# Performance work log

Hardware: AMD Instinct MI355X
Metric: run time of the kernel (lower is better)

The kernel has to match this reference:

```python
import jax, jax.numpy as jnp
import numpy as np

B, C, L = 4, 64, 4096

def setup_inputs() -> dict:
    key = jax.random.key(0)
    ks = jax.random.split(key, 7)
    s = 1.0 / np.sqrt(C)
    return {
        "x": jax.random.normal(ks[0], (B, C, L), dtype=jnp.float32),
        "wq": jax.random.uniform(ks[1], (C, C), jnp.float32, -s, s),
        "bq": jax.random.uniform(ks[2], (C,), jnp.float32, -s, s),
        "wk": jax.random.uniform(ks[3], (C, C), jnp.float32, -s, s),
        "bk": jax.random.uniform(ks[4], (C,), jnp.float32, -s, s),
        "wv": jax.random.uniform(ks[5], (C, C), jnp.float32, -s, s),
        "bv": jax.random.uniform(ks[6], (C,), jnp.float32, -s, s),
    }

def reference(x, wq, bq, wk, bk, wv, bv):
    # x: [B, C, L]; conv1d kernel-size-1 == per-position linear over channels.
    scale = jnp.sqrt(jnp.asarray(x.shape[1], x.dtype))
    # project and move to [B, L, C]
    q = jnp.einsum('oc,bcl->blo', wq, x) + bq  # [B, L, C]
    k = jnp.einsum('oc,bcl->blo', wk, x) + bk
    v = jnp.einsum('oc,bcl->blo', wv, x) + bv
    attn = jnp.einsum('bic,bjc->bij', q, k) / scale  # [B, L, L]
    attn = jax.nn.softmax(attn, axis=-1)
    out = jnp.einsum('bij,bjc->bic', attn, v)  # [B, L, C]
    return out.transpose(0, 2, 1) + x  # back to [B, C, L] with residual
```

## Files before the change

kernel.cpp:

```cpp
#include <hip/hip_runtime.h>
#include <hip/hip_bf16.h>

typedef float    f32x4  __attribute__((ext_vector_type(4)));
typedef float    f32x16 __attribute__((ext_vector_type(16)));
typedef short    s16x4  __attribute__((ext_vector_type(4)));
typedef short    s16x8  __attribute__((ext_vector_type(8)));
typedef unsigned u32x4  __attribute__((ext_vector_type(4)));
typedef __bf16   bf16x8 __attribute__((ext_vector_type(8)));

#define DEVI __device__ __forceinline__

DEVI short f2bf(float f) {
    unsigned u = __builtin_bit_cast(unsigned, f);
    u += 0x8000u;
    return (short)(u >> 16);
}
DEVI unsigned cvt_pk_bf16(float lo, float hi) {
#if defined(__HIP_DEVICE_COMPILE__)
    unsigned r;
    asm("v_cvt_pk_bf16_f32 %0, %1, %2" : "=v"(r) : "v"(lo), "v"(hi));
    return r;
#else
    return (unsigned)(unsigned short)f2bf(lo) | ((unsigned)(unsigned short)f2bf(hi) << 16);
#endif
}

DEVI float fast_exp2(float x) {
#if defined(__HIP_DEVICE_COMPILE__) && __has_builtin(__builtin_amdgcn_exp2f)
    return __builtin_amdgcn_exp2f(x);
#else
    return exp2f(x);
#endif
}

DEVI f32x4 mfma32(s16x8 a, s16x8 b, f32x4 c) {
#if defined(__HIP_DEVICE_COMPILE__) && __has_builtin(__builtin_amdgcn_mfma_f32_16x16x32_bf16)
    return __builtin_amdgcn_mfma_f32_16x16x32_bf16(
        __builtin_bit_cast(bf16x8, a), __builtin_bit_cast(bf16x8, b), c, 0, 0, 0);
#else
    asm volatile("v_mfma_f32_16x16x32_bf16 %0, %1, %2, %0" : "+v"(c) : "v"(a), "v"(b));
    return c;
#endif
}

DEVI f32x16 mfma3216(s16x8 a, s16x8 b, f32x16 c) {
#if defined(__HIP_DEVICE_COMPILE__) && __has_builtin(__builtin_amdgcn_mfma_f32_32x32x16_bf16)
    return __builtin_amdgcn_mfma_f32_32x32x16_bf16(
        __builtin_bit_cast(bf16x8, a), __builtin_bit_cast(bf16x8, b), c, 0, 0, 0);
#else
    asm volatile("v_mfma_f32_32x32x16_bf16 %0, %1, %2, %0" : "+v"(c) : "v"(a), "v"(b));
    return c;
#endif
}

DEVI void setprio1() {
#if defined(__HIP_DEVICE_COMPILE__)
    __builtin_amdgcn_s_setprio(1);
#endif
}
DEVI void setprio0() {
#if defined(__HIP_DEVICE_COMPILE__)
    __builtin_amdgcn_s_setprio(0);
#endif
}

DEVI void gld_lds16(const short* g, short* ldsb, int lane) {
#if defined(__HIP_DEVICE_COMPILE__) && __has_builtin(__builtin_amdgcn_global_load_lds)
    __builtin_amdgcn_global_load_lds(
        (const __attribute__((address_space(1))) void*)g,
        (__attribute__((address_space(3))) void*)ldsb, 16, 0, 0);
#else
    *reinterpret_cast<s16x8*>(ldsb + lane * 8) =
        *reinterpret_cast<const s16x8*>(g);
#endif
}

__global__ __launch_bounds__(512) void qkv_proj(
    const float* __restrict__ x,
    const float* __restrict__ wq, const float* __restrict__ bq,
    const float* __restrict__ wk, const float* __restrict__ bk,
    const float* __restrict__ wv, const float* __restrict__ bv,
    short* __restrict__ Qg, short* __restrict__ Kp, short* __restrict__ Vp)
{
    __shared__ short Xt[32 * 64];

    const int b  = blockIdx.x >> 7;
    const int l0 = (blockIdx.x & 127) * 32;
    const int t  = threadIdx.x;
    const float QS = 0.18033688011112042f;

    {
        const int c  = t & 63;
        const int lh = (t >> 6) * 4;
        const float* xr = x + ((size_t)b * 64 + c) * 4096 + l0 + lh;
        const float4 x0 = *reinterpret_cast<const float4*>(xr);
        float xv[4] = {x0.x, x0.y, x0.z, x0.w};
        #pragma unroll
        for (int i = 0; i < 4; ++i) {
            const int l = lh + i;
            Xt[l * 64 + (((c >> 3) ^ (l & 7)) * 8) + (c & 7)] = f2bf(xv[i]);
        }
    }

    const int lane = t & 63, w = t >> 6;
    const int g = lane >> 4, col = lane & 15;
    const int o0 = (w & 3) * 16;
    const int h  = w >> 2;

    s16x8 wqf[2], wkf[2], wvf[2];
    #pragma unroll
    for (int kc = 0; kc < 2; ++kc) {
        const int cb = 8 * g + 32 * kc;
        const float4 q0 = *reinterpret_cast<const float4*>(wq + (o0 + col) * 64 + cb);
        const float4 q1 = *reinterpret_cast<const float4*>(wq + (o0 + col) * 64 + cb + 4);
        const float4 k0 = *reinterpret_cast<const float4*>(wk + (o0 + col) * 64 + cb);
        const float4 k1 = *reinterpret_cast<const float4*>(wk + (o0 + col) * 64 + cb + 4);
        const float4 v0 = *reinterpret_cast<const float4*>(wv + (o0 + col) * 64 + cb);
        const float4 v1 = *reinterpret_cast<const float4*>(wv + (o0 + col) * 64 + cb + 4);
        wqf[kc][0] = f2bf(q0.x * QS); wqf[kc][1] = f2bf(q0.y * QS);
        wqf[kc][2] = f2bf(q0.z * QS); wqf[kc][3] = f2bf(q0.w * QS);
        wqf[kc][4] = f2bf(q1.x * QS); wqf[kc][5] = f2bf(q1.y * QS);
        wqf[kc][6] = f2bf(q1.z * QS); wqf[kc][7] = f2bf(q1.w * QS);
        wkf[kc][0] = f2bf(k0.x); wkf[kc][1] = f2bf(k0.y);
        wkf[kc][2] = f2bf(k0.z); wkf[kc][3] = f2bf(k0.w);
        wkf[kc][4] = f2bf(k1.x); wkf[kc][5] = f2bf(k1.y);
        wkf[kc][6] = f2bf(k1.z); wkf[kc][7] = f2bf(k1.w);
        wvf[kc][0] = f2bf(v0.x); wvf[kc][1] = f2bf(v0.y);
        wvf[kc][2] = f2bf(v0.z); wvf[kc][3] = f2bf(v0.w);
        wvf[kc][4] = f2bf(v1.x); wvf[kc][5] = f2bf(v1.y);
        wvf[kc][6] = f2bf(v1.z); wvf[kc][7] = f2bf(v1.w);
    }
    const f32x4 bq4 = *reinterpret_cast<const f32x4*>(bq + o0 + 4 * g);
    const f32x4 bk4 = *reinterpret_cast<const f32x4*>(bk + o0 + 4 * g);
    const float bvs = bv[o0 + col];

    __syncthreads();

    {
        const int row = h * 16 + col;
        const s16x8 xf0 = *reinterpret_cast<const s16x8*>(
            &Xt[row * 64 + ((g ^ (row & 7)) * 8)]);
        const s16x8 xf1 = *reinterpret_cast<const s16x8*>(
            &Xt[row * 64 + (((g + 4) ^ (row & 7)) * 8)]);

        f32x4 qa = bq4 * QS;
        qa = mfma32(wqf[0], xf0, qa);
        qa = mfma32(wqf[1], xf1, qa);
        f32x4 ka = bk4;
        ka = mfma32(wkf[0], xf0, ka);
        ka = mfma32(wkf[1], xf1, ka);
        f32x4 va = {bvs, bvs, bvs, bvs};
        va = mfma32(xf0, wvf[0], va);
        va = mfma32(xf1, wvf[1], va);

        s16x4 qs, ks;
        #pragma unroll
        for (int r = 0; r < 4; ++r) { qs[r] = f2bf(qa[r]); ks[r] = f2bf(ka[r]); }

        const int l  = l0 + row;
        const int d0 = o0 + 4 * g;
        *reinterpret_cast<s16x4*>(Qg + ((size_t)b * 4096 + l) * 64 + d0) = qs;

        {
            const int T  = l >> 6;
            const int rj = l & 63;
            const int off = rj * 64 + (((d0 >> 3) ^ (rj & 7)) << 3)
                          + ((d0 >> 2) & 1) * 4;
            *reinterpret_cast<s16x4*>(
                Kp + ((size_t)(b * 64 + T)) * 4096 + off) = ks;
        }

        {
            s16x4 vs;
            #pragma unroll
            for (int r = 0; r < 4; ++r) vs[r] = f2bf(va[r]);
            const int dV  = o0 + col;
            const int jgl = l0 + h * 16 + 4 * g;
            const int TV  = jgl >> 6;
            const int g4  = (jgl & 63) >> 2;
            const int p   = (g4 & 12) | ((g4 >> 1) & 1) | ((g4 & 1) << 1);
            const int off = dV * 64 + (((p >> 1) ^ (dV & 7)) << 3) + (p & 1) * 4;
            *reinterpret_cast<s16x4*>(
                Vp + ((size_t)(b * 64 + TV)) * 4096 + off) = vs;
        }
    }
}

__global__ __launch_bounds__(512, 2) void attn_fused(
    const short* __restrict__ Qg, const short* __restrict__ Kp,
    const short* __restrict__ Vp, const float* __restrict__ x,
    float* __restrict__ out)
{
    __shared__ short SM[65536];

    const int bid = blockIdx.x;
    const int wid = (bid & 7) * 32 + (bid >> 3);
    const int b   = wid >> 6;
    const int qt  = wid & 63;

    const int t    = threadIdx.x;
    const int w    = t >> 6;
    const int lane = t & 63;
    const int qi   = lane & 31;
    const int hi   = lane >> 5;
    const int rx   = qi & 7;
    const int kw   = w & 3;
    const int qw   = w >> 2;

    const int qglob = qt * 64 + qw * 32 + qi;

    s16x8 qf[4];
    {
        const short* qp = Qg + ((size_t)b * 4096 + qglob) * 64 + 8 * hi;
        qf[0] = *reinterpret_cast<const s16x8*>(qp);
        qf[1] = *reinterpret_cast<const s16x8*>(qp + 16);
        qf[2] = *reinterpret_cast<const s16x8*>(qp + 32);
        qf[3] = *reinterpret_cast<const s16x8*>(qp + 48);
    }

    const int ds = w & 3;
    const short* srcb = (w < 4)
        ? (Kp + ((size_t)(b * 64 + ds * 16)) * 4096 + lane * 8)
        : (Vp + ((size_t)(b * 64 + ds * 16)) * 4096 + lane * 8);
    short* ldsb = (w < 4) ? (SM + (ds * 2) * 4096)
                          : (SM + 32768 + (ds * 2) * 4096);

    {
        const short* s0 = srcb;
        short* l0p = ldsb;
        #pragma unroll
        for (int i = 0; i < 8; ++i)
            gld_lds16(s0 + i * 512, l0p + i * 512, lane);
    }
    __syncthreads();

    f32x16 oacc0 = {}, oacc1 = {};
    float lsum = 0.0f;

    #pragma unroll 2
    for (int tt = 0; tt < 16; ++tt) {
        const int cur = tt & 1;
        const short* Kl = SM + (kw * 2 + cur) * 4096;
        const short* Vl = SM + 32768 + (kw * 2 + cur) * 4096;

        if (tt < 15) {
            const short* s1 = srcb + (size_t)(tt + 1) * 4096;
            short* l1p = ldsb + (cur ^ 1) * 4096;
            #pragma unroll
            for (int i = 0; i < 8; ++i)
                gld_lds16(s1 + i * 512, l1p + i * 512, lane);
        }

        #pragma unroll
        for (int jb = 0; jb < 2; ++jb) {
            const short* kr  = Kl + (jb * 32 + qi) * 64;
            const short* vr0 = Vl + qi * 64;
            const short* vr1 = Vl + (32 + qi) * 64;

            f32x16 S = {};
            setprio1();
            #pragma unroll
            for (int m = 0; m < 4; ++m) {
                const s16x8 a = *reinterpret_cast<const s16x8*>(
                    kr + (((2 * m + hi) ^ rx) * 8));
                S = mfma3216(a, qf[m], S);
            }
            setprio0();

            const int sA0 = ((4 * jb + 0 + hi) ^ rx) * 8;
            const int sA1 = ((4 * jb + 2 + hi) ^ rx) * 8;
            const s16x8 va00 = *reinterpret_cast<const s16x8*>(vr0 + sA0);
            const s16x8 va10 = *reinterpret_cast<const s16x8*>(vr1 + sA0);
            const s16x8 va01 = *reinterpret_cast<const s16x8*>(vr0 + sA1);
            const s16x8 va11 = *reinterpret_cast<const s16x8*>(vr1 + sA1);

            unsigned Pu[8];
            float ps = 0.0f;
            #pragma unroll
            for (int i = 0; i < 8; ++i) {
                const float e0 = fast_exp2(S[2 * i]);
                const float e1 = fast_exp2(S[2 * i + 1]);
                ps += e0 + e1;
                Pu[i] = cvt_pk_bf16(e0, e1);
            }
            lsum += ps;
            const u32x4 w0 = {Pu[0], Pu[1], Pu[2], Pu[3]};
            const u32x4 w1 = {Pu[4], Pu[5], Pu[6], Pu[7]};

            setprio1();
            oacc0 = mfma3216(va00, __builtin_bit_cast(s16x8, w0), oacc0);
            oacc1 = mfma3216(va10, __builtin_bit_cast(s16x8, w0), oacc1);
            oacc0 = mfma3216(va01, __builtin_bit_cast(s16x8, w1), oacc0);
            oacc1 = mfma3216(va11, __builtin_bit_cast(s16x8, w1), oacc1);
            setprio0();
        }

        __syncthreads();
    }

    const float ltot = lsum + __shfl_xor(lsum, 32);

    float* Of = reinterpret_cast<float*>(SM);
    float* Lf = Of + 256 * 65;
    {
        const int rowb = (kw * 64 + qw * 32 + qi) * 65;
        #pragma unroll
        for (int db = 0; db < 2; ++db) {
            const f32x16 oa = db ? oacc1 : oacc0;
            #pragma unroll
            for (int r = 0; r < 16; ++r) {
                const int d = (r & 3) + 8 * (r >> 2) + 4 * hi + 32 * db;
                Of[rowb + d] = oa[r];
            }
        }
        if (hi == 0) Lf[kw * 64 + qw * 32 + qi] = ltot;
    }
    __syncthreads();

    {
        const int d  = t >> 3;
        const int q8 = (t & 7) * 8;
        float res[8];
        #pragma unroll
        for (int i = 0; i < 8; ++i) {
            const int rb = q8 + i;
            const float L = Lf[rb] + Lf[64 + rb] + Lf[128 + rb] + Lf[192 + rb];
            const float o = Of[(rb)       * 65 + d] + Of[(64 + rb)  * 65 + d] +
                            Of[(128 + rb) * 65 + d] + Of[(192 + rb) * 65 + d];
            res[i] = o / L;
        }
        const size_t ob = ((size_t)b * 64 + d) * 4096 + qt * 64 + q8;
        const float4 x0 = *reinterpret_cast<const float4*>(x + ob);
        const float4 x1 = *reinterpret_cast<const float4*>(x + ob + 4);
        float4 o0 = {res[0] + x0.x, res[1] + x0.y, res[2] + x0.z, res[3] + x0.w};
        float4 o1 = {res[4] + x1.x, res[5] + x1.y, res[6] + x1.z, res[7] + x1.w};
        *reinterpret_cast<float4*>(out + ob)     = o0;
        *reinterpret_cast<float4*>(out + ob + 4) = o1;
    }
}

extern "C" void kernel_launch(void* const* d_in, const int* in_sizes, int n_in,
                              void* d_out, int out_size, void* d_ws, size_t ws_size,
                              hipStream_t stream) {
    const float* x  = (const float*)d_in[0];
    const float* wq = (const float*)d_in[1];
    const float* bq = (const float*)d_in[2];
    const float* wk = (const float*)d_in[3];
    const float* bk = (const float*)d_in[4];
    const float* wv = (const float*)d_in[5];
    const float* bv = (const float*)d_in[6];
    float* out = (float*)d_out;

    short* Qg = reinterpret_cast<short*>(d_ws);
    short* Kp = Qg + (size_t)4 * 4096 * 64;
    short* Vp = Kp + (size_t)4 * 4096 * 64;

    qkv_proj<<<dim3(512), dim3(512), 0, stream>>>(x, wq, bq, wk, bk, wv, bv, Qg, Kp, Vp);
    attn_fused<<<dim3(256), dim3(512), 0, stream>>>(Qg, Kp, Vp, x, out);
}
```

Measured before the change: 39.18 us.

## Split key tile across waves with both query halves per wave, bf16 partial reduction

Each wave now computes scores for both 32-query halves against one 32-key half of the tile, so every K fragment loaded from shared memory feeds two sets of MFMAs instead of each wave owning one query half and looping over both key halves. This cuts LDS reads of K per tile and gives more independent MFMA chains per wave, at the cost of more accumulator registers (four output accumulators plus two score tiles). The cross-wave reduction is widened to 8 partials per query, and those partials are stored to shared memory as bf16 to fit. This adds rounding error in the output sum and changes the epilogue store pattern to strided scalar writes.

```diff
diff --git a/kernel.cpp b/kernel.cpp
--- a/kernel.cpp
+++ b/kernel.cpp
@@ -5,6 +5,7 @@
 typedef float    f32x16 __attribute__((ext_vector_type(16)));
 typedef short    s16x4  __attribute__((ext_vector_type(4)));
 typedef short    s16x8  __attribute__((ext_vector_type(8)));
+typedef unsigned u32x2  __attribute__((ext_vector_type(2)));
 typedef unsigned u32x4  __attribute__((ext_vector_type(4)));
 typedef __bf16   bf16x8 __attribute__((ext_vector_type(8)));
 
@@ -14,6 +15,9 @@
     unsigned u = __builtin_bit_cast(unsigned, f);
     u += 0x8000u;
     return (short)(u >> 16);
+}
+DEVI float bf2f(short s) {
+    return __builtin_bit_cast(float, ((unsigned)(unsigned short)s) << 16);
 }
 DEVI unsigned cvt_pk_bf16(float lo, float hi) {
 #if defined(__HIP_DEVICE_COMPILE__)
@@ -205,17 +209,16 @@
     const int hi   = lane >> 5;
     const int rx   = qi & 7;
     const int kw   = w & 3;
-    const int qw   = w >> 2;
-
-    const int qglob = qt * 64 + qw * 32 + qi;
-
-    s16x8 qf[4];
-    {
-        const short* qp = Qg + ((size_t)b * 4096 + qglob) * 64 + 8 * hi;
-        qf[0] = *reinterpret_cast<const s16x8*>(qp);
-        qf[1] = *reinterpret_cast<const s16x8*>(qp + 16);
-        qf[2] = *reinterpret_cast<const s16x8*>(qp + 32);
-        qf[3] = *reinterpret_cast<const s16x8*>(qp + 48);
+    const int h2   = w >> 2;
+
+    s16x8 qf[2][4];
+    #pragma unroll
+    for (int qs = 0; qs < 2; ++qs) {
+        const short* qp = Qg + ((size_t)b * 4096 + qt * 64 + qs * 32 + qi) * 64 + 8 * hi;
+        qf[qs][0] = *reinterpret_cast<const s16x8*>(qp);
+        qf[qs][1] = *reinterpret_cast<const s16x8*>(qp + 16);
+        qf[qs][2] = *reinterpret_cast<const s16x8*>(qp + 32);
+        qf[qs][3] = *reinterpret_cast<const s16x8*>(qp + 48);
     }
 
     const int ds = w & 3;
@@ -234,8 +237,8 @@
     }
     __syncthreads();
 
-    f32x16 oacc0 = {}, oacc1 = {};
-    float lsum = 0.0f;
+    f32x16 oa00 = {}, oa01 = {}, oa10 = {}, oa11 = {};
+    float ls0 = 0.0f, ls1 = 0.0f;
 
     #pragma unroll 2
     for (int tt = 0; tt < 16; ++tt) {
@@ -251,91 +254,117 @@
                 gld_lds16(s1 + i * 512, l1p + i * 512, lane);
         }
 
-        #pragma unroll
-        for (int jb = 0; jb < 2; ++jb) {
-            const short* kr  = Kl + (jb * 32 + qi) * 64;
-            const short* vr0 = Vl + qi * 64;
-            const short* vr1 = Vl + (32 + qi) * 64;
-
-            f32x16 S = {};
-            setprio1();
+        const short* kr = Kl + (h2 * 32 + qi) * 64;
+        s16x8 ka[4];
+        #pragma unroll
+        for (int m = 0; m < 4; ++m)
+            ka[m] = *reinterpret_cast<const s16x8*>(kr + (((2 * m + hi) ^ rx) * 8));
+
+        f32x16 S0 = {}, S1 = {};
+        setprio1();
+        #pragma unroll
+        for (int m = 0; m < 4; ++m) S0 = mfma3216(ka[m], qf[0][m], S0);
+        #pragma unroll
+        for (int m = 0; m < 4; ++m) S1 = mfma3216(ka[m], qf[1][m], S1);
+        setprio0();
+
+        const short* vr0 = Vl + qi * 64;
+        const short* vr1 = Vl + (32 + qi) * 64;
+        const int sA0 = ((4 * h2 + 0 + hi) ^ rx) * 8;
+        const int sA1 = ((4 * h2 + 2 + hi) ^ rx) * 8;
+        const s16x8 va00 = *reinterpret_cast<const s16x8*>(vr0 + sA0);
+        const s16x8 va10 = *reinterpret_cast<const s16x8*>(vr1 + sA0);
+        const s16x8 va01 = *reinterpret_cast<const s16x8*>(vr0 + sA1);
+        const s16x8 va11 = *reinterpret_cast<const s16x8*>(vr1 + sA1);
+
+        unsigned P0[8], P1[8];
+        float ps0 = 0.0f, ps1 = 0.0f;
+        #pragma unroll
+        for (int i = 0; i < 8; ++i) {
+            const float e0 = fast_exp2(S0[2 * i]);
+            const float e1 = fast_exp2(S0[2 * i + 1]);
+            ps0 += e0 + e1;
+            P0[i] = cvt_pk_bf16(e0, e1);
+            const float f0 = fast_exp2(S1[2 * i]);
+            const float f1 = fast_exp2(S1[2 * i + 1]);
+            ps1 += f0 + f1;
+            P1[i] = cvt_pk_bf16(f0, f1);
+        }
+        ls0 += ps0; ls1 += ps1;
+        const u32x4 w00 = {P0[0], P0[1], P0[2], P0[3]};
+        const u32x4 w01 = {P0[4], P0[5], P0[6], P0[7]};
+        const u32x4 w10 = {P1[0], P1[1], P1[2], P1[3]};
+        const u32x4 w11 = {P1[4], P1[5], P1[6], P1[7]};
+
+        setprio1();
+        oa00 = mfma3216(va00, __builtin_bit_cast(s16x8, w00), oa00);
+        oa01 = mfma3216(va10, __builtin_bit_cast(s16x8, w00), oa01);
+        oa10 = mfma3216(va00, __builtin_bit_cast(s16x8, w10), oa10);
+        oa11 = mfma3216(va10, __builtin_bit_cast(s16x8, w10), oa11);
+        oa00 = mfma3216(va01, __builtin_bit_cast(s16x8, w01), oa00);
+        oa01 = mfma3216(va11, __builtin_bit_cast(s16x8, w01), oa01);
+        oa10 = mfma3216(va01, __builtin_bit_cast(s16x8, w11), oa10);
+        oa11 = mfma3216(va11, __builtin_bit_cast(s16x8, w11), oa11);
+        setprio0();
+
+        __syncthreads();
+    }
+
+    const float lt0 = ls0 + __shfl_xor(ls0, 32);
+    const float lt1 = ls1 + __shfl_xor(ls1, 32);
+
+    short* Po = SM;
+    float* Lf = reinterpret_cast<float*>(SM + 512 * 68);
+    {
+        const int row0 = w * 64 + qi;
+        const int row1 = w * 64 + 32 + qi;
+        #pragma unroll
+        for (int db = 0; db < 2; ++db) {
+            const f32x16 a0 = db ? oa01 : oa00;
+            const f32x16 a1 = db ? oa11 : oa10;
             #pragma unroll
-            for (int m = 0; m < 4; ++m) {
-                const s16x8 a = *reinterpret_cast<const s16x8*>(
-                    kr + (((2 * m + hi) ^ rx) * 8));
-                S = mfma3216(a, qf[m], S);
+            for (int rq = 0; rq < 4; ++rq) {
+                const int dbase = 8 * rq + 4 * hi + 32 * db;
+                u32x2 pk0, pk1;
+                pk0[0] = cvt_pk_bf16(a0[4 * rq + 0], a0[4 * rq + 1]);
+                pk0[1] = cvt_pk_bf16(a0[4 * rq + 2], a0[4 * rq + 3]);
+                pk1[0] = cvt_pk_bf16(a1[4 * rq + 0], a1[4 * rq + 1]);
+                pk1[1] = cvt_pk_bf16(a1[4 * rq + 2], a1[4 * rq + 3]);
+                *reinterpret_cast<u32x2*>(&Po[row0 * 68 + dbase]) = pk0;
+                *reinterpret_cast<u32x2*>(&Po[row1 * 68 + dbase]) = pk1;
             }
-            setprio0();
-
-            const int sA0 = ((4 * jb + 0 + hi) ^ rx) * 8;
-            const int sA1 = ((4 * jb + 2 + hi) ^ rx) * 8;
-            const s16x8 va00 = *reinterpret_cast<const s16x8*>(vr0 + sA0);
-            const s16x8 va10 = *reinterpret_cast<const s16x8*>(vr1 + sA0);
-            const s16x8 va01 = *reinterpret_cast<const s16x8*>(vr0 + sA1);
-            const s16x8 va11 = *reinterpret_cast<const s16x8*>(vr1 + sA1);
-
-            unsigned Pu[8];
-            float ps = 0.0f;
+        }
+        if (hi == 0) {
+            Lf[row0] = lt0;
+            Lf[row1] = lt1;
+        }
+    }
+    __syncthreads();
+
+    {
+        const int q  = t & 63;
+        const int dst = (t >> 6) * 8;
+        float acc[8] = {};
+        float L = 0.0f;
+        #pragma unroll
+        for (int s = 0; s < 8; ++s) {
+            const int row = s * 64 + q;
+            L += Lf[row];
+            const s16x4 o0 = *reinterpret_cast<const s16x4*>(&Po[row * 68 + dst]);
+            const s16x4 o1 = *reinterpret_cast<const s16x4*>(&Po[row * 68 + dst + 4]);
             #pragma unroll
-            for (int i = 0; i < 8; ++i) {
-                const float e0 = fast_exp2(S[2 * i]);
-                const float e1 = fast_exp2(S[2 * i + 1]);
-                ps += e0 + e1;
-                Pu[i] = cvt_pk_bf16(e0, e1);
+            for (int i = 0; i < 4; ++i) {
+                acc[i]     += bf2f(o0[i]);
+                acc[4 + i] += bf2f(o1[i]);
             }
-            lsum += ps;
-            const u32x4 w0 = {Pu[0], Pu[1], Pu[2], Pu[3]};
-            const u32x4 w1 = {Pu[4], Pu[5], Pu[6], Pu[7]};
-
-            setprio1();
-            oacc0 = mfma3216(va00, __builtin_bit_cast(s16x8, w0), oacc0);
-            oacc1 = mfma3216(va10, __builtin_bit_cast(s16x8, w0), oacc1);
-            oacc0 = mfma3216(va01, __builtin_bit_cast(s16x8, w1), oacc0);
-            oacc1 = mfma3216(va11, __builtin_bit_cast(s16x8, w1), oacc1);
-            setprio0();
-        }
-
-        __syncthreads();
-    }
-
-    const float ltot = lsum + __shfl_xor(lsum, 32);
-
-    float* Of = reinterpret_cast<float*>(SM);
-    float* Lf = Of + 256 * 65;
-    {
-        const int rowb = (kw * 64 + qw * 32 + qi) * 65;
-        #pragma unroll
-        for (int db = 0; db < 2; ++db) {
-            const f32x16 oa = db ? oacc1 : oacc0;
-            #pragma unroll
-            for (int r = 0; r < 16; ++r) {
-                const int d = (r & 3) + 8 * (r >> 2) + 4 * hi + 32 * db;
-                Of[rowb + d] = oa[r];
-            }
-        }
-        if (hi == 0) Lf[kw * 64 + qw * 32 + qi] = ltot;
-    }
-    __syncthreads();
-
-    {
-        const int d  = t >> 3;
-        const int q8 = (t & 7) * 8;
-        float res[8];
+        }
+        const float rL = 1.0f / L;
+        const size_t ob = ((size_t)b * 64 + dst) * 4096 + qt * 64 + q;
         #pragma unroll
         for (int i = 0; i < 8; ++i) {
-            const int rb = q8 + i;
-            const float L = Lf[rb] + Lf[64 + rb] + Lf[128 + rb] + Lf[192 + rb];
-            const float o = Of[(rb)       * 65 + d] + Of[(64 + rb)  * 65 + d] +
-                            Of[(128 + rb) * 65 + d] + Of[(192 + rb) * 65 + d];
-            res[i] = o / L;
-        }
-        const size_t ob = ((size_t)b * 64 + d) * 4096 + qt * 64 + q8;
-        const float4 x0 = *reinterpret_cast<const float4*>(x + ob);
-        const float4 x1 = *reinterpret_cast<const float4*>(x + ob + 4);
-        float4 o0 = {res[0] + x0.x, res[1] + x0.y, res[2] + x0.z, res[3] + x0.w};
-        float4 o1 = {res[4] + x1.x, res[5] + x1.y, res[6] + x1.z, res[7] + x1.w};
-        *reinterpret_cast<float4*>(out + ob)     = o0;
-        *reinterpret_cast<float4*>(out + ob + 4) = o1;
+            const size_t idx = ob + (size_t)i * 4096;
+            out[idx] = fmaf(acc[i], rL, x[idx]);
+        }
     }
 }
 
```

Measured after the change: 39.40 us. No clear change (+0.6%).

## Triple-buffer K/V tiles with vmcnt waits and re-split waves across key halves

Applied to the files above, without the earlier changes.

The attention kernel now streams 32 half-tiles of K/V through a three-slot LDS ring and prefetches two tiles ahead. Each iteration uses a partial s_waitcnt vmcnt plus a raw barrier instead of a full __syncthreads, so global-to-LDS loads can stay in flight across iterations. Wave roles change: each wave handles one key half of one stream per iteration, and LDS shrinks to 96KB. The epilogue stores partial outputs as bf16 and reduces them with per-column coalesced stores, which adds bf16 rounding error in the cross-wave reduction.

```diff
diff --git a/kernel.cpp b/kernel.cpp
--- a/kernel.cpp
+++ b/kernel.cpp
@@ -5,6 +5,7 @@
 typedef float    f32x16 __attribute__((ext_vector_type(16)));
 typedef short    s16x4  __attribute__((ext_vector_type(4)));
 typedef short    s16x8  __attribute__((ext_vector_type(8)));
+typedef unsigned u32x2  __attribute__((ext_vector_type(2)));
 typedef unsigned u32x4  __attribute__((ext_vector_type(4)));
 typedef __bf16   bf16x8 __attribute__((ext_vector_type(8)));
 
@@ -14,6 +15,9 @@
     unsigned u = __builtin_bit_cast(unsigned, f);
     u += 0x8000u;
     return (short)(u >> 16);
+}
+DEVI float bf2f(short s) {
+    return __builtin_bit_cast(float, ((unsigned)(unsigned short)s) << 16);
 }
 DEVI unsigned cvt_pk_bf16(float lo, float hi) {
 #if defined(__HIP_DEVICE_COMPILE__)
@@ -63,15 +67,32 @@
     __builtin_amdgcn_s_setprio(0);
 #endif
 }
-
-DEVI void gld_lds16(const short* g, short* ldsb, int lane) {
+DEVI void vm_wait4() {
+#if defined(__HIP_DEVICE_COMPILE__)
+    asm volatile("s_waitcnt vmcnt(4)" ::: "memory");
+#endif
+}
+DEVI void vm_wait0() {
+#if defined(__HIP_DEVICE_COMPILE__)
+    asm volatile("s_waitcnt vmcnt(0)" ::: "memory");
+#endif
+}
+DEVI void raw_barrier() {
+#if defined(__HIP_DEVICE_COMPILE__)
+    __builtin_amdgcn_s_barrier();
+#endif
+}
+DEVI void sched_fence() {
+#if defined(__HIP_DEVICE_COMPILE__)
+    __builtin_amdgcn_sched_barrier(0);
+#endif
+}
+
+DEVI void gld_lds16(const short* g, short* ldsb) {
 #if defined(__HIP_DEVICE_COMPILE__) && __has_builtin(__builtin_amdgcn_global_load_lds)
     __builtin_amdgcn_global_load_lds(
         (const __attribute__((address_space(1))) void*)g,
         (__attribute__((address_space(3))) void*)ldsb, 16, 0, 0);
-#else
-    *reinterpret_cast<s16x8*>(ldsb + lane * 8) =
-        *reinterpret_cast<const s16x8*>(g);
 #endif
 }
 
@@ -191,7 +212,7 @@
     const short* __restrict__ Vp, const float* __restrict__ x,
     float* __restrict__ out)
 {
-    __shared__ short SM[65536];
+    __shared__ short SM[49152];
 
     const int bid = blockIdx.x;
     const int wid = (bid & 7) * 32 + (bid >> 3);
@@ -204,138 +225,150 @@
     const int qi   = lane & 31;
     const int hi   = lane >> 5;
     const int rx   = qi & 7;
-    const int kw   = w & 3;
-    const int qw   = w >> 2;
-
-    const int qglob = qt * 64 + qw * 32 + qi;
+    const int s    = w & 1;
+    const int h2   = (w >> 1) & 1;
+    const int qs   = w >> 2;
 
     s16x8 qf[4];
     {
-        const short* qp = Qg + ((size_t)b * 4096 + qglob) * 64 + 8 * hi;
+        const short* qp = Qg + ((size_t)b * 4096 + qt * 64 + qs * 32 + qi) * 64 + 8 * hi;
         qf[0] = *reinterpret_cast<const s16x8*>(qp);
         qf[1] = *reinterpret_cast<const s16x8*>(qp + 16);
         qf[2] = *reinterpret_cast<const s16x8*>(qp + 32);
         qf[3] = *reinterpret_cast<const s16x8*>(qp + 48);
     }
 
-    const int ds = w & 3;
-    const short* srcb = (w < 4)
-        ? (Kp + ((size_t)(b * 64 + ds * 16)) * 4096 + lane * 8)
-        : (Vp + ((size_t)(b * 64 + ds * 16)) * 4096 + lane * 8);
-    short* ldsb = (w < 4) ? (SM + (ds * 2) * 4096)
-                          : (SM + 32768 + (ds * 2) * 4096);
-
-    {
-        const short* s0 = srcb;
-        short* l0p = ldsb;
-        #pragma unroll
-        for (int i = 0; i < 8; ++i)
-            gld_lds16(s0 + i * 512, l0p + i * 512, lane);
-    }
-    __syncthreads();
+    const int part = w >> 1;
+    const int poff = (part & 1) * 2048;
+    const short* dsrc = ((part < 2) ? Kp : Vp)
+        + ((size_t)(b * 64 + s * 32)) * 4096 + poff + lane * 8;
+    short* dbase = SM + ((part < 2) ? 0 : 24576) + s * 3 * 4096 + poff;
+
+    #pragma unroll
+    for (int i = 0; i < 4; ++i) gld_lds16(dsrc + i * 512, dbase + i * 512);
+    #pragma unroll
+    for (int i = 0; i < 4; ++i)
+        gld_lds16(dsrc + 4096 + i * 512, dbase + 4096 + i * 512);
+    vm_wait4();
+    raw_barrier();
+    sched_fence();
 
     f32x16 oacc0 = {}, oacc1 = {};
     float lsum = 0.0f;
 
+    const short* Kc = SM + s * 3 * 4096;
+    const short* Vc = SM + 24576 + s * 3 * 4096;
+
+    int cb = 0;
     #pragma unroll 2
-    for (int tt = 0; tt < 16; ++tt) {
-        const int cur = tt & 1;
-        const short* Kl = SM + (kw * 2 + cur) * 4096;
-        const short* Vl = SM + 32768 + (kw * 2 + cur) * 4096;
-
-        if (tt < 15) {
-            const short* s1 = srcb + (size_t)(tt + 1) * 4096;
-            short* l1p = ldsb + (cur ^ 1) * 4096;
+    for (int tt = 0; tt < 32; ++tt) {
+        if (tt < 30) {
+            const int ib = (cb >= 1) ? (cb - 1) : 2;
+            const short* gsrc = dsrc + (size_t)(tt + 2) * 4096;
+            short* ldst = dbase + ib * 4096;
             #pragma unroll
-            for (int i = 0; i < 8; ++i)
-                gld_lds16(s1 + i * 512, l1p + i * 512, lane);
-        }
-
-        #pragma unroll
-        for (int jb = 0; jb < 2; ++jb) {
-            const short* kr  = Kl + (jb * 32 + qi) * 64;
-            const short* vr0 = Vl + qi * 64;
-            const short* vr1 = Vl + (32 + qi) * 64;
-
-            f32x16 S = {};
-            setprio1();
-            #pragma unroll
-            for (int m = 0; m < 4; ++m) {
-                const s16x8 a = *reinterpret_cast<const s16x8*>(
-                    kr + (((2 * m + hi) ^ rx) * 8));
-                S = mfma3216(a, qf[m], S);
-            }
-            setprio0();
-
-            const int sA0 = ((4 * jb + 0 + hi) ^ rx) * 8;
-            const int sA1 = ((4 * jb + 2 + hi) ^ rx) * 8;
-            const s16x8 va00 = *reinterpret_cast<const s16x8*>(vr0 + sA0);
-            const s16x8 va10 = *reinterpret_cast<const s16x8*>(vr1 + sA0);
-            const s16x8 va01 = *reinterpret_cast<const s16x8*>(vr0 + sA1);
-            const s16x8 va11 = *reinterpret_cast<const s16x8*>(vr1 + sA1);
-
-            unsigned Pu[8];
-            float ps = 0.0f;
-            #pragma unroll
-            for (int i = 0; i < 8; ++i) {
-                const float e0 = fast_exp2(S[2 * i]);
-                const float e1 = fast_exp2(S[2 * i + 1]);
-                ps += e0 + e1;
-                Pu[i] = cvt_pk_bf16(e0, e1);
-            }
-            lsum += ps;
-            const u32x4 w0 = {Pu[0], Pu[1], Pu[2], Pu[3]};
-            const u32x4 w1 = {Pu[4], Pu[5], Pu[6], Pu[7]};
-
-            setprio1();
-            oacc0 = mfma3216(va00, __builtin_bit_cast(s16x8, w0), oacc0);
-            oacc1 = mfma3216(va10, __builtin_bit_cast(s16x8, w0), oacc1);
-            oacc0 = mfma3216(va01, __builtin_bit_cast(s16x8, w1), oacc0);
-            oacc1 = mfma3216(va11, __builtin_bit_cast(s16x8, w1), oacc1);
-            setprio0();
-        }
-
-        __syncthreads();
+            for (int i = 0; i < 4; ++i) gld_lds16(gsrc + i * 512, ldst + i * 512);
+        }
+
+        const short* Kl = Kc + cb * 4096;
+        const short* Vl = Vc + cb * 4096;
+
+        const short* kr = Kl + (h2 * 32 + qi) * 64;
+        f32x16 S = {};
+        setprio1();
+        #pragma unroll
+        for (int m = 0; m < 4; ++m) {
+            const s16x8 a = *reinterpret_cast<const s16x8*>(
+                kr + (((2 * m + hi) ^ rx) * 8));
+            S = mfma3216(a, qf[m], S);
+        }
+        setprio0();
+
+        const short* vr0 = Vl + qi * 64;
+        const short* vr1 = Vl + (32 + qi) * 64;
+        const int sA0 = ((4 * h2 + 0 + hi) ^ rx) * 8;
+        const int sA1 = ((4 * h2 + 2 + hi) ^ rx) * 8;
+        const s16x8 va00 = *reinterpret_cast<const s16x8*>(vr0 + sA0);
+        const s16x8 va10 = *reinterpret_cast<const s16x8*>(vr1 + sA0);
+        const s16x8 va01 = *reinterpret_cast<const s16x8*>(vr0 + sA1);
+        const s16x8 va11 = *reinterpret_cast<const s16x8*>(vr1 + sA1);
+
+        unsigned Pu[8];
+        float ps = 0.0f;
+        #pragma unroll
+        for (int i = 0; i < 8; ++i) {
+            const float e0 = fast_exp2(S[2 * i]);
+            const float e1 = fast_exp2(S[2 * i + 1]);
+            ps += e0 + e1;
+            Pu[i] = cvt_pk_bf16(e0, e1);
+        }
+        lsum += ps;
+        const u32x4 w0 = {Pu[0], Pu[1], Pu[2], Pu[3]};
+        const u32x4 w1 = {Pu[4], Pu[5], Pu[6], Pu[7]};
+
+        setprio1();
+        oacc0 = mfma3216(va00, __builtin_bit_cast(s16x8, w0), oacc0);
+        oacc1 = mfma3216(va10, __builtin_bit_cast(s16x8, w0), oacc1);
+        oacc0 = mfma3216(va01, __builtin_bit_cast(s16x8, w1), oacc0);
+        oacc1 = mfma3216(va11, __builtin_bit_cast(s16x8, w1), oacc1);
+        setprio0();
+
+        if (tt < 31) {
+            if (tt < 30) vm_wait4();
+            else         vm_wait0();
+            raw_barrier();
+            sched_fence();
+        }
+        cb = (cb >= 2) ? 0 : (cb + 1);
     }
 
     const float ltot = lsum + __shfl_xor(lsum, 32);
 
-    float* Of = reinterpret_cast<float*>(SM);
-    float* Lf = Of + 256 * 65;
-    {
-        const int rowb = (kw * 64 + qw * 32 + qi) * 65;
+    __syncthreads();
+    short* Po = SM;
+    float* Lf = reinterpret_cast<float*>(SM + 256 * 68);
+    {
+        const int row = (w & 3) * 64 + qs * 32 + qi;
         #pragma unroll
         for (int db = 0; db < 2; ++db) {
             const f32x16 oa = db ? oacc1 : oacc0;
             #pragma unroll
-            for (int r = 0; r < 16; ++r) {
-                const int d = (r & 3) + 8 * (r >> 2) + 4 * hi + 32 * db;
-                Of[rowb + d] = oa[r];
+            for (int rq = 0; rq < 4; ++rq) {
+                u32x2 pk;
+                pk[0] = cvt_pk_bf16(oa[4 * rq + 0], oa[4 * rq + 1]);
+                pk[1] = cvt_pk_bf16(oa[4 * rq + 2], oa[4 * rq + 3]);
+                const int dbase2 = 8 * rq + 4 * hi + 32 * db;
+                *reinterpret_cast<u32x2*>(&Po[row * 68 + dbase2]) = pk;
             }
         }
-        if (hi == 0) Lf[kw * 64 + qw * 32 + qi] = ltot;
+        if (hi == 0) Lf[row] = ltot;
     }
     __syncthreads();
 
     {
-        const int d  = t >> 3;
-        const int q8 = (t & 7) * 8;
-        float res[8];
+        const int q  = t & 63;
+        const int dst = (t >> 6) * 8;
+        float acc[8] = {};
+        float L = 0.0f;
+        #pragma unroll
+        for (int sh = 0; sh < 4; ++sh) {
+            const int row = sh * 64 + q;
+            L += Lf[row];
+            const s16x4 o0 = *reinterpret_cast<const s16x4*>(&Po[row * 68 + dst]);
+            const s16x4 o1 = *reinterpret_cast<const s16x4*>(&Po[row * 68 + dst + 4]);
+            #pragma unroll
+            for (int i = 0; i < 4; ++i) {
+                acc[i]     += bf2f(o0[i]);
+                acc[4 + i] += bf2f(o1[i]);
+            }
+        }
+        const float rL = 1.0f / L;
+        const size_t ob = ((size_t)b * 64 + dst) * 4096 + qt * 64 + q;
         #pragma unroll
         for (int i = 0; i < 8; ++i) {
-            const int rb = q8 + i;
-            const float L = Lf[rb] + Lf[64 + rb] + Lf[128 + rb] + Lf[192 + rb];
-            const float o = Of[(rb)       * 65 + d] + Of[(64 + rb)  * 65 + d] +
-                            Of[(128 + rb) * 65 + d] + Of[(192 + rb) * 65 + d];
-            res[i] = o / L;
-        }
-        const size_t ob = ((size_t)b * 64 + d) * 4096 + qt * 64 + q8;
-        const float4 x0 = *reinterpret_cast<const float4*>(x + ob);
-        const float4 x1 = *reinterpret_cast<const float4*>(x + ob + 4);
-        float4 o0 = {res[0] + x0.x, res[1] + x0.y, res[2] + x0.z, res[3] + x0.w};
-        float4 o1 = {res[4] + x1.x, res[5] + x1.y, res[6] + x1.z, res[7] + x1.w};
-        *reinterpret_cast<float4*>(out + ob)     = o0;
-        *reinterpret_cast<float4*>(out + ob + 4) = o1;
+            const size_t idx = ob + (size_t)i * 4096;
+            out[idx] = fmaf(acc[i], rL, x[idx]);
+        }
     }
 }
 
```

Result: slower. 41.01 us (+4.7%).
